# Performance work log

Hardware: AMD Instinct MI355X
Metric: run time of the kernel (lower is better)

Reference implementation:

```python
import jax, jax.numpy as jnp
import numpy as np

B, L, D_MODEL, D_FF, N_EXPERTS, TOP_K = 32, 256, 512, 2048, 8, 2
EPS = 1e-9


def setup_inputs() -> dict:
    key = jax.random.key(0)
    ks = jax.random.split(key, 7)
    scale1 = 1.0 / np.sqrt(D_MODEL)
    scale2 = 1.0 / np.sqrt(D_FF)
    return {
        "cycle_curve_data": jax.random.normal(ks[0], (B, L, D_MODEL), jnp.float32),
        "logits": jax.random.normal(ks[1], (B, N_EXPERTS), jnp.float32),
        "moe_masks": jax.random.randint(ks[2], (B, N_EXPERTS), 0, 2, jnp.int32),
        "W1": jax.random.normal(ks[3], (N_EXPERTS, D_MODEL, D_FF), jnp.float32) * scale1,
        "b1": jax.random.normal(ks[4], (N_EXPERTS, D_FF), jnp.float32) * scale1,
        "W2": jax.random.normal(ks[5], (N_EXPERTS, D_FF, D_MODEL), jnp.float32) * scale2,
        "b2": jax.random.normal(ks[6], (N_EXPERTS, D_MODEL), jnp.float32) * scale2,
    }


def _gates(logits, moe_masks):
    # softmax over experts, zero out unavailable experts, keep top-k, renormalize
    mask = (moe_masks == 1).astype(logits.dtype)               # [B, E]
    p = jax.nn.softmax(logits, axis=1) * mask                  # [B, E]
    _, idx = jax.lax.top_k(p, TOP_K)                           # [B, K]
    topk_mask = jnp.zeros_like(p).at[jnp.arange(p.shape[0])[:, None], idx].set(1.0)
    p = p * topk_mask
    return p / (jnp.sum(p, axis=1, keepdims=True) + EPS)       # [B, E]


def reference(cycle_curve_data, logits, moe_masks, W1, b1, W2, b2):
    gates = _gates(logits, moe_masks)                          # [B, E]
    x = cycle_curve_data                                       # [B, L, D]
    # dense equivalent of per-expert gather -> MLP -> gate-weighted scatter-combine
    h = jnp.einsum("bld,edf->eblf", x, W1) + b1[:, None, None, :]   # [E,B,L,F]
    h = jax.nn.gelu(h, approximate=False)
    out = jnp.einsum("be,eblf,efd->bld", gates, h, W2)
    out = out + jnp.einsum("be,ed->bd", gates, b2)[:, None, :]      # [B,L,D]
    return out
```

## Files before the change

### kernel.cpp

```cpp
#include <hip/hip_runtime.h>

#define B_SZ 32
#define L_SZ 256
#define D_SZ 512
#define F_SZ 2048
#define E_SZ 8
#define P_SZ 64
#define BK2  32

typedef __attribute__((ext_vector_type(8)))  short bf16x8;
typedef __attribute__((ext_vector_type(16))) float f32x16;

__device__ __forceinline__ unsigned short f2bf(float f) {
  unsigned int u = __builtin_bit_cast(unsigned int, f);
  u += 0x7fffu + ((u >> 16) & 1u);
  return (unsigned short)(u >> 16);
}

__device__ __forceinline__ void async16(const void* g, void* l) {
  __builtin_amdgcn_global_load_lds(
      (const __attribute__((address_space(1))) unsigned int*)g,
      (__attribute__((address_space(3))) unsigned int*)l, 16, 0, 0);
}

__device__ __forceinline__ float gelu_f(float x) {
  float a = fabsf(x) * 0.70710678118654752f;
  float t = __builtin_amdgcn_rcpf(1.0f + 0.3275911f * a);
  float y = t * (0.254829592f +
            t * (-0.284496736f +
            t * (1.421413741f +
            t * (-1.453152027f +
            t * 1.061405429f))));
  float e = __expf(-a * a);
  float erf_abs = 1.0f - y * e;
  float erf_v = (x < 0.f) ? -erf_abs : erf_abs;
  return 0.5f * x * (1.0f + erf_v);
}

template <int NT>
__device__ __forceinline__ void transpose_tile(
    const float* __restrict__ ip, unsigned short* __restrict__ op,
    int R, int C, int r0, int c0, float* tile, int tid) {
  int tx = tid & 63, ty = tid >> 6;
  constexpr int RY = NT / 64;
#pragma unroll
  for (int i = 0; i < 64 / RY; ++i) {
    int r = i * RY + ty;
    tile[r * 65 + tx] = ip[(size_t)(r0 + r) * C + c0 + tx];
  }
  __syncthreads();
#pragma unroll
  for (int uu = 0; uu < 1024 / NT; ++uu) {
    int u = uu * NT + tid;
    int cc = u >> 4, q = u & 15;
    ushort4 o;
    o.x = f2bf(tile[(q * 4 + 0) * 65 + cc]);
    o.y = f2bf(tile[(q * 4 + 1) * 65 + cc]);
    o.z = f2bf(tile[(q * 4 + 2) * 65 + cc]);
    o.w = f2bf(tile[(q * 4 + 3) * 65 + cc]);
    *(ushort4*)(op + (size_t)(c0 + cc) * R + r0 + q * 4) = o;
  }
}

#define PREP_CONV_BLKS 4096
#define PREP_TR_BLKS   2048
#define PREP_TOTAL     (1 + PREP_CONV_BLKS + PREP_TR_BLKS)

__global__ __launch_bounds__(256) void prep_kernel(
    const float* __restrict__ logits, const int* __restrict__ masks,
    const float* __restrict__ x,
    const float* __restrict__ W1,
    int* __restrict__ sel_e, float* __restrict__ sel_g,
    unsigned short* __restrict__ xb,
    unsigned short* __restrict__ w1t) {
  __shared__ float tile[64 * 65];
  int blk = blockIdx.x;
  int tid = threadIdx.x;

  if (blk == 0) {
    int b = tid;
    if (b >= B_SZ) return;
    float lg[E_SZ], p[E_SZ];
    float mx = -1e30f;
    for (int e = 0; e < E_SZ; ++e) { lg[e] = logits[b * E_SZ + e]; mx = fmaxf(mx, lg[e]); }
    float s = 0.f;
    for (int e = 0; e < E_SZ; ++e) { p[e] = expf(lg[e] - mx); s += p[e]; }
    for (int e = 0; e < E_SZ; ++e) p[e] = (masks[b * E_SZ + e] == 1) ? (p[e] / s) : 0.f;
    int i0 = 0, i1 = 1; float v0 = -1.f, v1 = -1.f;
    for (int e = 0; e < E_SZ; ++e) {
      float v = p[e];
      if (v > v0)      { v1 = v0; i1 = i0; v0 = v; i0 = e; }
      else if (v > v1) { v1 = v;  i1 = e; }
    }
    float den = v0 + v1 + 1e-9f;
    sel_e[2 * b] = i0;  sel_e[2 * b + 1] = i1;
    sel_g[2 * b] = v0 / den;
    sel_g[2 * b + 1] = v1 / den;
    return;
  }
  blk -= 1;

  if (blk < PREP_CONV_BLKS) {
    int i = blk * 256 + tid;
    float4 v = ((const float4*)x)[i];
    ushort4 o;
    o.x = f2bf(v.x); o.y = f2bf(v.y); o.z = f2bf(v.z); o.w = f2bf(v.w);
    ((ushort4*)xb)[i] = o;
    return;
  }
  blk -= PREP_CONV_BLKS;

  int z = blk >> 8;
  int rem = blk & 255;
  int tr = rem >> 5, tc = rem & 31;
  transpose_tile<256>(W1 + (size_t)z * D_SZ * F_SZ, w1t + (size_t)z * D_SZ * F_SZ,
                      D_SZ, F_SZ, tr * 64, tc * 64, tile, tid);
}

__global__ __launch_bounds__(512, 4) void moe_gemm1(
    const unsigned short* __restrict__ Xb,
    const unsigned short* __restrict__ W1t,
    const float* __restrict__ b1,
    const int* __restrict__ sel_e,
    unsigned short* __restrict__ H,
    const float* __restrict__ W2,
    unsigned short* __restrict__ w2t) {
  __shared__ __align__(16) char smem[49152];
  int tid = threadIdx.x;
  int lin = blockIdx.x;

  if (lin >= 1024) {
    int blk = lin - 1024;
    int z = blk >> 8;
    int rem = blk & 255;
    int tr = rem >> 3, tc = rem & 7;
    transpose_tile<512>(W2 + (size_t)z * F_SZ * D_SZ, w2t + (size_t)z * F_SZ * D_SZ,
                        F_SZ, D_SZ, tr * 64, tc * 64, (float*)smem, tid);
    return;
  }

  unsigned short* As = (unsigned short*)smem;
  unsigned short* Bs = (unsigned short*)(smem + 16384);

  int f  = lin & 7;
  int l0 = ((lin >> 3) & 1) * 128;
  int p  = lin >> 4;
  int f0 = f * 256;
  int b  = p >> 1;
  int e  = sel_e[p];

  int lane = tid & 63;
  int w = tid >> 6;
  int wm = w & 1, wn = w >> 1;
  int m32 = lane & 31, kh = lane >> 5;
  int sw = (m32 >> 1) & 3;

  const unsigned short* Abase = Xb  + ((size_t)b * L_SZ + l0) * D_SZ;
  const unsigned short* Bbase = W1t + ((size_t)e * F_SZ + f0) * D_SZ;

  int sa   = tid;
  int rowa = sa >> 2,  ka  = ((sa  & 3) ^ ((rowa >> 1) & 3)) * 8;
  int sb1  = tid + 512;
  int rowb = sb1 >> 2, kb1 = ((sb1 & 3) ^ ((rowb >> 1) & 3)) * 8;

  const size_t aoffA  = (size_t)rowa * D_SZ + ka;
  const size_t aoffB1 = (size_t)rowb * D_SZ + kb1;

  f32x16 acc[2][2] = {};

#define G1_COMPUTE(CB)                                                       \
  _Pragma("unroll")                                                          \
  for (int s = 0; s < 2; ++s) {                                              \
    int ko = ((((s << 1) | kh) ^ sw) << 3);                                  \
    bf16x8 a0  = *(const bf16x8*)&As[(CB) * 4096 + (wm * 64 +      m32) * BK2 + ko]; \
    bf16x8 a1  = *(const bf16x8*)&As[(CB) * 4096 + (wm * 64 + 32 + m32) * BK2 + ko]; \
    bf16x8 b0  = *(const bf16x8*)&Bs[(CB) * 8192 + (wn * 64 +      m32) * BK2 + ko]; \
    bf16x8 b1f = *(const bf16x8*)&Bs[(CB) * 8192 + (wn * 64 + 32 + m32) * BK2 + ko]; \
    acc[0][0] = __builtin_amdgcn_mfma_f32_32x32x16_bf16(a0, b0,  acc[0][0], 0, 0, 0); \
    acc[0][1] = __builtin_amdgcn_mfma_f32_32x32x16_bf16(a0, b1f, acc[0][1], 0, 0, 0); \
    acc[1][0] = __builtin_amdgcn_mfma_f32_32x32x16_bf16(a1, b0,  acc[1][0], 0, 0, 0); \
    acc[1][1] = __builtin_amdgcn_mfma_f32_32x32x16_bf16(a1, b1f, acc[1][1], 0, 0, 0); \
  }

  async16(Abase + aoffA,  &As[sa * 8]);
  async16(Bbase + aoffA,  &Bs[sa * 8]);
  async16(Bbase + aoffB1, &Bs[sb1 * 8]);
  __syncthreads();

#pragma unroll 2
  for (int t = 0; t < 15; ++t) {
    int cb = t & 1, nb = cb ^ 1;
    int kk = (t + 1) * BK2;
    async16(Abase + aoffA  + kk, &As[nb * 4096 + sa * 8]);
    async16(Bbase + aoffA  + kk, &Bs[nb * 8192 + sa * 8]);
    async16(Bbase + aoffB1 + kk, &Bs[nb * 8192 + sb1 * 8]);
    G1_COMPUTE(cb)
    __syncthreads();
  }
  G1_COMPUTE(1)
#undef G1_COMPUTE

  float b1v[2];
#pragma unroll
  for (int tj = 0; tj < 2; ++tj)
    b1v[tj] = b1[e * F_SZ + f0 + wn * 64 + tj * 32 + m32];

  unsigned short* Hp = H + ((size_t)p * L_SZ + l0) * F_SZ + f0;
#pragma unroll
  for (int ti = 0; ti < 2; ++ti)
#pragma unroll
    for (int tj = 0; tj < 2; ++tj) {
      int col = wn * 64 + tj * 32 + m32;
#pragma unroll
      for (int r = 0; r < 16; ++r) {
        int row = wm * 64 + ti * 32 + (r & 3) + 8 * (r >> 2) + 4 * kh;
        Hp[(size_t)row * F_SZ + col] = f2bf(gelu_f(acc[ti][tj][r] + b1v[tj]));
      }
    }
}

__global__ __launch_bounds__(128, 2) void moe_gemm2(
    const unsigned short* __restrict__ H,
    const unsigned short* __restrict__ W2t,
    const float* __restrict__ b2,
    const int* __restrict__ sel_e,
    const float* __restrict__ sel_g,
    float* __restrict__ part,
    float* __restrict__ Out) {
  __shared__ __align__(16) unsigned short As[2][128 * BK2];
  __shared__ __align__(16) unsigned short Bs[2][64 * BK2];

  int lin = blockIdx.x;
  int q   = lin & 7;
  int d   = (lin >> 3) & 7;
  int g8  = lin >> 6;
  int gg  = g8 * 8 + q;
  int p   = gg >> 1;
  int l0  = (gg & 1) * 128;
  int d0  = d * 64;
  int b   = p >> 1;
  int e   = sel_e[p];
  float g = sel_g[p];

  int tid = threadIdx.x;
  int lane = tid & 63;
  int wm = tid >> 6;
  int m32 = lane & 31, kh = lane >> 5;
  int sw = (m32 >> 1) & 3;

  const unsigned short* Abase = H   + ((size_t)p * L_SZ + l0) * F_SZ;
  const unsigned short* Bbase = W2t + ((size_t)e * D_SZ + d0) * F_SZ;

  int    saA[4]; size_t aoffA[4];
#pragma unroll
  for (int j = 0; j < 4; ++j) {
    int s = tid + j * 128;
    int row = s >> 2, ks = ((s & 3) ^ ((row >> 1) & 3)) * 8;
    saA[j] = s; aoffA[j] = (size_t)row * F_SZ + ks;
  }
  int    saB[2]; size_t aoffB[2];
#pragma unroll
  for (int j = 0; j < 2; ++j) {
    int s = tid + j * 128;
    int row = s >> 2, ks = ((s & 3) ^ ((row >> 1) & 3)) * 8;
    saB[j] = s; aoffB[j] = (size_t)row * F_SZ + ks;
  }

  f32x16 acc[2][2] = {};

  for (int k0 = 0; k0 < F_SZ; k0 += 2 * BK2) {
#pragma unroll
    for (int h = 0; h < 2; ++h) {
      int kk = k0 + h * BK2;
#pragma unroll
      for (int j = 0; j < 4; ++j)
        async16(Abase + aoffA[j] + kk, &As[h][saA[j] * 8]);
#pragma unroll
      for (int j = 0; j < 2; ++j)
        async16(Bbase + aoffB[j] + kk, &Bs[h][saB[j] * 8]);
    }
    __syncthreads();
#pragma unroll
    for (int h = 0; h < 2; ++h)
#pragma unroll
      for (int s = 0; s < 2; ++s) {
        int ko = (((s << 1) | kh) ^ sw) << 3;
        bf16x8 a0  = *(const bf16x8*)&As[h][(wm * 64 +      m32) * BK2 + ko];
        bf16x8 a1  = *(const bf16x8*)&As[h][(wm * 64 + 32 + m32) * BK2 + ko];
        bf16x8 b0  = *(const bf16x8*)&Bs[h][(          m32) * BK2 + ko];
        bf16x8 b1f = *(const bf16x8*)&Bs[h][(     32 + m32) * BK2 + ko];
        acc[0][0] = __builtin_amdgcn_mfma_f32_32x32x16_bf16(a0, b0,  acc[0][0], 0, 0, 0);
        acc[0][1] = __builtin_amdgcn_mfma_f32_32x32x16_bf16(a0, b1f, acc[0][1], 0, 0, 0);
        acc[1][0] = __builtin_amdgcn_mfma_f32_32x32x16_bf16(a1, b0,  acc[1][0], 0, 0, 0);
        acc[1][1] = __builtin_amdgcn_mfma_f32_32x32x16_bf16(a1, b1f, acc[1][1], 0, 0, 0);
      }
    __syncthreads();
  }

  float bias[2] = {0.f, 0.f};
  if (p & 1) {
    int e0 = sel_e[2 * b], e1 = sel_e[2 * b + 1];
    float g0 = sel_g[2 * b], g1 = sel_g[2 * b + 1];
#pragma unroll
    for (int tj = 0; tj < 2; ++tj) {
      int dd = d0 + tj * 32 + m32;
      bias[tj] = g0 * b2[e0 * D_SZ + dd] + g1 * b2[e1 * D_SZ + dd];
    }
  }
  float* dst = (p & 1) ? Out : part;
  float* Op = dst + ((size_t)b * L_SZ + l0) * D_SZ + d0;
#pragma unroll
  for (int ti = 0; ti < 2; ++ti)
#pragma unroll
    for (int tj = 0; tj < 2; ++tj) {
      int col = tj * 32 + m32;
#pragma unroll
      for (int r = 0; r < 16; ++r) {
        int row = wm * 64 + ti * 32 + (r & 3) + 8 * (r >> 2) + 4 * kh;
        Op[(size_t)row * D_SZ + col] = g * acc[ti][tj][r] + bias[tj];
      }
    }
}

__global__ __launch_bounds__(256) void combine_kernel(
    const float* __restrict__ part, float* __restrict__ Out) {
  int i = blockIdx.x * 256 + threadIdx.x;
  float4 pv = ((const float4*)part)[i];
  float4 o  = ((float4*)Out)[i];
  o.x += pv.x; o.y += pv.y; o.z += pv.z; o.w += pv.w;
  ((float4*)Out)[i] = o;
}

extern "C" void kernel_launch(void* const* d_in, const int* in_sizes, int n_in,
                              void* d_out, int out_size, void* d_ws, size_t ws_size,
                              hipStream_t stream) {
  const float* x      = (const float*)d_in[0];
  const float* logits = (const float*)d_in[1];
  const int*   masks  = (const int*)d_in[2];
  const float* W1     = (const float*)d_in[3];
  const float* b1     = (const float*)d_in[4];
  const float* W2     = (const float*)d_in[5];
  const float* b2     = (const float*)d_in[6];
  float* out = (float*)d_out;

  char* ws = (char*)d_ws;
  int*   sel_e = (int*)ws;
  float* sel_g = (float*)(ws + 256);
  unsigned short* xb  = (unsigned short*)(ws + 1024);
  unsigned short* w1t = xb  + (size_t)B_SZ * L_SZ * D_SZ;
  unsigned short* w2t = w1t + (size_t)E_SZ * F_SZ * D_SZ;
  unsigned short* Hbuf = w2t + (size_t)E_SZ * D_SZ * F_SZ;
  float* part = (float*)(ws + 1024);

  prep_kernel<<<PREP_TOTAL, 256, 0, stream>>>(logits, masks, x, W1,
                                              sel_e, sel_g, xb, w1t);
  moe_gemm1<<<3072, 512, 0, stream>>>(xb, w1t, b1, sel_e, Hbuf, W2, w2t);
  moe_gemm2<<<1024, 128, 0, stream>>>(Hbuf, w2t, b2, sel_e, sel_g, part, out);
  combine_kernel<<<(B_SZ * L_SZ * D_SZ / 4) / 256, 256, 0, stream>>>(part, out);
}
```

Measured before the change: 242.7 us.

## Double-buffer the down-projection GEMM K loop to overlap loads with MFMA

Replaces the load-two-K-slices-then-compute loop in the second GEMM with a software pipeline. Each step prefetches the next 32-wide K slice into the alternate LDS buffer while MFMAs consume the current one, with one barrier per step instead of two. This is meant to hide global-to-LDS latency behind matrix math. The cost is twice as many loop iterations, each with less work, and the correctness of the buffer handoff now depends on the barrier also waiting for the async LDS loads to finish.

```diff
diff --git a/kernel.cpp b/kernel.cpp
--- a/kernel.cpp
+++ b/kernel.cpp
@@ -268,34 +268,41 @@
 
   f32x16 acc[2][2] = {};
 
-  for (int k0 = 0; k0 < F_SZ; k0 += 2 * BK2) {
-#pragma unroll
-    for (int h = 0; h < 2; ++h) {
-      int kk = k0 + h * BK2;
-#pragma unroll
-      for (int j = 0; j < 4; ++j)
-        async16(Abase + aoffA[j] + kk, &As[h][saA[j] * 8]);
-#pragma unroll
-      for (int j = 0; j < 2; ++j)
-        async16(Bbase + aoffB[j] + kk, &Bs[h][saB[j] * 8]);
-    }
+#define G2_COMPUTE(CB)                                                       \
+  _Pragma("unroll")                                                          \
+  for (int s = 0; s < 2; ++s) {                            \
+    int ko = (((s << 1) | kh) ^ sw) << 3;                                    \
+    bf16x8 a0  = *(const bf16x8*)&As[CB][(wm * 64 +      m32) * BK2 + ko];   \
+    bf16x8 a1  = *(const bf16x8*)&As[CB][(wm * 64 + 32 + m32) * BK2 + ko];   \
+    bf16x8 b0  = *(const bf16x8*)&Bs[CB][(          m32) * BK2 + ko];        \
+    bf16x8 b1f = *(const bf16x8*)&Bs[CB][(     32 + m32) * BK2 + ko];        \
+    acc[0][0] = __builtin_amdgcn_mfma_f32_32x32x16_bf16(a0, b0,  acc[0][0], 0, 0, 0); \
+    acc[0][1] = __builtin_amdgcn_mfma_f32_32x32x16_bf16(a0, b1f, acc[0][1], 0, 0, 0); \
+    acc[1][0] = __builtin_amdgcn_mfma_f32_32x32x16_bf16(a1, b0,  acc[1][0], 0, 0, 0); \
+    acc[1][1] = __builtin_amdgcn_mfma_f32_32x32x16_bf16(a1, b1f, acc[1][1], 0, 0, 0); \
+  }
+
+#pragma unroll
+  for (int j = 0; j < 4; ++j) async16(Abase + aoffA[j], &As[0][saA[j] * 8]);
+#pragma unroll
+  for (int j = 0; j < 2; ++j) async16(Bbase + aoffB[j], &Bs[0][saB[j] * 8]);
+  __syncthreads();
+
+#pragma unroll 2
+  for (int t = 0; t < 63; ++t) {
+    int cb = t & 1, nb = cb ^ 1;
+    int kk = (t + 1) * BK2;
+#pragma unroll
+    for (int j = 0; j < 4; ++j)
+      async16(Abase + aoffA[j] + kk, &As[nb][saA[j] * 8]);
+#pragma unroll
+    for (int j = 0; j < 2; ++j)
+      async16(Bbase + aoffB[j] + kk, &Bs[nb][saB[j] * 8]);
+    G2_COMPUTE(cb)
     __syncthreads();
-#pragma unroll
-    for (int h = 0; h < 2; ++h)
-#pragma unroll
-      for (int s = 0; s < 2; ++s) {
-        int ko = (((s << 1) | kh) ^ sw) << 3;
-        bf16x8 a0  = *(const bf16x8*)&As[h][(wm * 64 +      m32) * BK2 + ko];
-        bf16x8 a1  = *(const bf16x8*)&As[h][(wm * 64 + 32 + m32) * BK2 + ko];
-        bf16x8 b0  = *(const bf16x8*)&Bs[h][(          m32) * BK2 + ko];
-        bf16x8 b1f = *(const bf16x8*)&Bs[h][(     32 + m32) * BK2 + ko];
-        acc[0][0] = __builtin_amdgcn_mfma_f32_32x32x16_bf16(a0, b0,  acc[0][0], 0, 0, 0);
-        acc[0][1] = __builtin_amdgcn_mfma_f32_32x32x16_bf16(a0, b1f, acc[0][1], 0, 0, 0);
-        acc[1][0] = __builtin_amdgcn_mfma_f32_32x32x16_bf16(a1, b0,  acc[1][0], 0, 0, 0);
-        acc[1][1] = __builtin_amdgcn_mfma_f32_32x32x16_bf16(a1, b1f, acc[1][1], 0, 0, 0);
-      }
-    __syncthreads();
-  }
+  }
+  G2_COMPUTE(1)
+#undef G2_COMPUTE
 
   float bias[2] = {0.f, 0.f};
   if (p & 1) {
```

Measured after the change: 259.2 us. +6.8%, slower.
